# Kernel tuning notes

Measured on AMD Instinct MI355X. Metric: run time of the kernel, lower is better.

## Reference

```python
import jax, jax.numpy as jnp
import numpy as np
import math

DIMS, HEAD = 1024, 16
HD = DIMS // HEAD          # 64
B, CTX = 4, 1024
MAX_ITER, THRESH = 3, 0.5  # temp=1.0 -> q temperature scaling branch is skipped (as in torch)
LOG10_21 = math.log10(1.0 + 4000.0 / 200.0)


def _freq_angles(c):
    # compute_freqs_base: 0.2*(10**linspace(0, log10(21), d/2) - 1), custom_freqs = 36000/220 * base
    d2 = HD // 2
    mel = 10.0 ** jnp.linspace(0.0, LOG10_21, d2) - 1.0
    freqs = (36000.0 / 220.0) * (200.0 * mel / 1000.0)        # [d2]
    t = jnp.arange(c, dtype=jnp.float32)
    return t[:, None] * freqs[None, :]                          # [c, d2]


def _rope(x, ang):
    # lucidrains rotary_embedding_torch convention: interleaved pairs (x0,x1),(x2,x3),...
    x1, x2 = x[..., 0::2], x[..., 1::2]
    cos, sin = jnp.cos(ang), jnp.sin(ang)
    out = jnp.stack([x1 * cos - x2 * sin, x1 * sin + x2 * cos], axis=-1)
    return out.reshape(x.shape)


def _rms(x, w):
    eps = jnp.finfo(x.dtype).eps  # torch nn.RMSNorm eps=None default
    return x * jax.lax.rsqrt(jnp.mean(jnp.square(x), -1, keepdims=True) + eps) * w


def _sdpa(q, k, v):
    # mask is always None in this module's forward -> non-causal SDPA
    s = jnp.einsum('bhqd,bhkd->bhqk', q, k) / math.sqrt(q.shape[-1])
    return jnp.einsum('bhqk,bhkd->bhqd', jax.nn.softmax(s, -1), v)


def _focus(x, xa, P):
    # x: [b, cq, D] queries, xa: [b, ck, D] keys/values. In our configs cq == ck == eff_span.
    b, cq, D = x.shape
    ck = xa.shape[1]
    q = _rms(x, P['wq_norm']) @ P['Wq'] + P['bq']
    q = q.reshape(b, cq, HEAD, HD).transpose(0, 2, 1, 3)                 # b h c d
    kv = _rms(xa, P['wkv_norm']) @ P['Wkv'] + P['bkv']
    kv = kv.reshape(b, ck, 2, HEAD, HD).transpose(2, 0, 3, 1, 4)         # kv b h c d
    k, v = kv[0], kv[1]
    q = _rope(q, _freq_angles(cq))
    k = _rope(k, _freq_angles(ck))

    e = min(cq, ck)  # static; equals cq in all call sites here
    curq, kc, vc = q, k[:, :, :e], v[:, :, :e]
    prev = jnp.zeros_like(q)
    attn_out = jnp.zeros_like(q)
    done = jnp.asarray(False)
    for it in range(MAX_ITER):
        # torch: q/k/v re-projected from current state EVERY iteration (k,v compound)
        qp = curq[:, :, :e] @ P['Wlq'] + P['blq']
        kp = kc @ P['Wlk'] + P['blk']
        vp = vc @ P['Wlv'] + P['blv']
        attn = _sdpa(_rms(qp, P['wln']), _rms(kp, P['wln']), vp)         # == iter_out since e == cq
        diff = jnp.mean(jnp.abs(attn - prev))
        stop = (diff < THRESH) & (it > 0) & (~done)
        attn_out = jnp.where(done, attn_out, attn)  # on the break iteration attn_out = iter_out
        done = done | stop
        curq = jnp.where(done, curq, curq + attn)
        prev = jnp.where(done, prev, attn)
        kc = jnp.where(done, kc, kp)
        vc = jnp.where(done, vc, vp)
    return attn_out.transpose(0, 2, 1, 3).reshape(b, cq, D)             # b c (h d)


def _slide(x, P):
    # win_size = head_dim; only the first win_size keys of each span are ever used
    b, ctx, D = x.shape
    w = HD
    off = w // HEAD                       # span_len - win_size
    nwin = ctx // w                       # ctx chosen as a multiple of w
    starts = jnp.maximum(jnp.arange(nwin) * w - off, 0)
    kidx = starts[:, None] + jnp.arange(w)[None, :]                      # [nwin, w]
    qwin = x.reshape(b, nwin, w, D).transpose(1, 0, 2, 3)                # [nwin, b, w, D]
    kwin = x[:, kidx, :].transpose(1, 0, 2, 3)                           # [nwin, b, w, D]
    outw = jax.vmap(lambda xq, xk: _focus(xq, xk, P))(qwin, kwin)
    return outw.transpose(1, 0, 2, 3).reshape(b, ctx, D)


def _forward(x, xa, P):
    xw = _slide(x, P)
    xaw = _slide(xa, P)
    out = _focus(xw, xaw, P)
    return out @ P['Wo'] + P['bo']        # Dropout(0.01) is identity in eval


def setup_inputs() -> dict:
    key = jax.random.key(0)
    ks = jax.random.split(key, 8)
    s = 0.02
    f32 = jnp.float32
    return {
        'x': jax.random.normal(ks[0], (B, CTX, DIMS), f32),
        'xa': jax.random.normal(ks[1], (B, CTX, DIMS), f32),
        'wq_norm': jnp.ones((DIMS,), f32),
        'Wq': jax.random.normal(ks[2], (DIMS, DIMS), f32) * s,
        'bq': jnp.zeros((DIMS,), f32),
        'wkv_norm': jnp.ones((DIMS,), f32),
        'Wkv': jax.random.normal(ks[3], (DIMS, 2 * DIMS), f32) * s,
        'bkv': jnp.zeros((2 * DIMS,), f32),
        'wln': jnp.ones((HD,), f32),
        'Wlq': jax.random.normal(ks[4], (HD, HD), f32) * s,
        'blq': jnp.zeros((HD,), f32),
        'Wlk': jax.random.normal(ks[5], (HD, HD), f32) * s,
        'blk': jnp.zeros((HD,), f32),
        'Wlv': jax.random.normal(ks[6], (HD, HD), f32) * s,
        'blv': jnp.zeros((HD,), f32),
        'Wo': jax.random.normal(ks[7], (DIMS, DIMS), f32) * s,
        'bo': jnp.zeros((DIMS,), f32),
    }


def reference(x, xa, wq_norm, Wq, bq, wkv_norm, Wkv, bkv, wln, Wlq, blq, Wlk, blk, Wlv, blv, Wo, bo):
    P = dict(wq_norm=wq_norm, Wq=Wq, bq=bq, wkv_norm=wkv_norm, Wkv=Wkv, bkv=bkv, wln=wln,
             Wlq=Wlq, blq=blq, Wlk=Wlk, blk=blk, Wlv=Wlv, blv=blv, Wo=Wo, bo=bo)
    return _forward(x, xa, P)
```

## Files before the change

### kernel.cpp

```cpp
#include <hip/hip_runtime.h>
#include <math.h>

#define TPB 256

static __device__ __forceinline__ float4 mk4(float a, float b, float c, float d) {
  float4 r; r.x = a; r.y = b; r.z = c; r.w = d; return r;
}

static __device__ __forceinline__ float4 ld4s(const float* buf, int row, int ch) {
  return *(const float4*)&buf[(row << 6) + (((ch ^ (row >> 2)) & 15) << 2)];
}
static __device__ __forceinline__ void st4s(float* buf, int row, int ch, float4 v) {
  *(float4*)&buf[(row << 6) + (((ch ^ (row >> 2)) & 15) << 2)] = v;
}

__global__ __launch_bounds__(TPB) void k_tables(float* __restrict__ cosb,
                                                float* __restrict__ sinb) {
  int gid = blockIdx.x * TPB + threadIdx.x;
  if (gid >= 1024 * 32) return;
  int t = gid >> 5, j = gid & 31;
  const double Ld = 1.3222192947339193;
  float Lf = (float)Ld;
  float mlog;
  if (j == 31) {
    mlog = Lf;
  } else {
    float stepf = (float)((double)j / 31.0);
    mlog = (float)((double)Lf * (double)stepf);
  }
  float p = (float)pow(10.0, (double)mlog);
  float mel = p - 1.0f;
  float t2 = (200.0f * mel) / 1000.0f;
  float freq = 163.63636363636363f * t2;
  float ang = (float)t * freq;
  double a = (double)ang;
  cosb[gid] = (float)cos(a);
  sinb[gid] = (float)sin(a);
}

__global__ __launch_bounds__(TPB) void k_rowinv(const float* __restrict__ X,
                                                float* __restrict__ inv) {
  __shared__ float red[4];
  int row = blockIdx.x;
  int tid = threadIdx.x;
  float4 v = *(const float4*)(X + (size_t)row * 1024 + tid * 4);
  float ss = v.x * v.x + v.y * v.y + v.z * v.z + v.w * v.w;
#pragma unroll
  for (int m = 1; m < 64; m <<= 1) ss += __shfl_xor(ss, m);
  if ((tid & 63) == 0) red[tid >> 6] = ss;
  __syncthreads();
  if (tid == 0) {
    float s = ((red[0] + red[1]) + (red[2] + red[3]));
    float mm = s * (1.0f / 1024.0f) + 1.1920928955078125e-7f;
    inv[row] = (float)(1.0 / sqrt((double)mm));
  }
}

__global__ __launch_bounds__(TPB) void k_gemm128(
    const float* __restrict__ X, const float* __restrict__ inv,
    const float* __restrict__ wn, const float* __restrict__ W,
    const float* __restrict__ bias, float* __restrict__ o0,
    float* __restrict__ o1, int N, int mode) {
  __shared__ float As[16][132];
  __shared__ float Bs[16][132];
  int tid = threadIdx.x;
  int bx = blockIdx.x, by = blockIdx.y;
  int tx = tid & 15, ty = tid >> 4;
  float c[8][8];
#pragma unroll
  for (int i = 0; i < 8; ++i)
#pragma unroll
    for (int j = 0; j < 8; ++j) c[i][j] = 0.0f;

  int arow = tid >> 1;
  float sA = 1.0f;
  if (inv) sA = inv[by * 128 + arow];
  const float* Xrow = X + (size_t)(by * 128 + arow) * 1024;

  for (int k0 = 0; k0 < 1024; k0 += 16) {
#pragma unroll
    for (int u = 0; u < 2; ++u) {
      int kq = ((tid & 1) * 2 + u) * 4;
      float4 a4 = *(const float4*)(Xrow + k0 + kq);
      if (wn) {
        float4 w4 = *(const float4*)(wn + k0 + kq);
        a4.x *= w4.x; a4.y *= w4.y; a4.z *= w4.z; a4.w *= w4.w;
      }
      a4.x *= sA; a4.y *= sA; a4.z *= sA; a4.w *= sA;
      As[kq + 0][arow] = a4.x;
      As[kq + 1][arow] = a4.y;
      As[kq + 2][arow] = a4.z;
      As[kq + 3][arow] = a4.w;
    }
#pragma unroll
    for (int u = 0; u < 2; ++u) {
      int kr = tid >> 4;
      int c4 = ((tid & 15) * 2 + u) * 4;
      *(float4*)&Bs[kr][c4] =
          *(const float4*)(W + (size_t)(k0 + kr) * N + bx * 128 + c4);
    }
    __syncthreads();
#pragma unroll
    for (int kk = 0; kk < 16; ++kk) {
      float4 a0 = *(const float4*)&As[kk][ty * 4];
      float4 a1 = *(const float4*)&As[kk][64 + ty * 4];
      float4 b0 = *(const float4*)&Bs[kk][tx * 4];
      float4 b1 = *(const float4*)&Bs[kk][64 + tx * 4];
      float av[8] = {a0.x, a0.y, a0.z, a0.w, a1.x, a1.y, a1.z, a1.w};
      float bv[8] = {b0.x, b0.y, b0.z, b0.w, b1.x, b1.y, b1.z, b1.w};
#pragma unroll
      for (int i = 0; i < 8; ++i)
#pragma unroll
        for (int j = 0; j < 8; ++j) c[i][j] += av[i] * bv[j];
    }
    __syncthreads();
  }

#pragma unroll
  for (int jh = 0; jh < 2; ++jh) {
    int colbase = bx * 128 + jh * 64 + tx * 4;
    float4 bb = {0.f, 0.f, 0.f, 0.f};
    if (bias) bb = *(const float4*)(bias + colbase);
#pragma unroll
    for (int ih = 0; ih < 2; ++ih) {
#pragma unroll
      for (int i2 = 0; i2 < 4; ++i2) {
        int row = by * 128 + ih * 64 + ty * 4 + i2;
        int ci = ih * 4 + i2;
        float4 o;
        o.x = c[ci][jh * 4 + 0] + bb.x;
        o.y = c[ci][jh * 4 + 1] + bb.y;
        o.z = c[ci][jh * 4 + 2] + bb.z;
        o.w = c[ci][jh * 4 + 3] + bb.w;
        if (mode == 0) {
          *(float4*)(o0 + (size_t)row * N + colbase) = o;
        } else {
          int b = row >> 10, t = row & 1023;
          float* dst = o0;
          int cc = colbase;
          if (mode == 2 && colbase >= 1024) { dst = o1; cc = colbase - 1024; }
          int ch = cc >> 6, d = cc & 63;
          *(float4*)(dst + ((size_t)((b * 16 + ch) * 1024 + t)) * 64 + d) = o;
        }
      }
    }
  }
}

__global__ __launch_bounds__(TPB) void k_rope(float* __restrict__ A, int mask,
                                              const float* __restrict__ cosb,
                                              const float* __restrict__ sinb) {
  int gid = blockIdx.x * TPB + threadIdx.x;
  int j = gid & 31;
  int row = gid >> 5;
  int t = row & 1023;
  int aidx = ((t & mask) << 5) + j;
  float cc = cosb[aidx], sn = sinb[aidx];
  size_t base = (size_t)row * 64;
  float x1 = A[base + 2 * j], x2 = A[base + 2 * j + 1];
  A[base + 2 * j] = x1 * cc - x2 * sn;
  A[base + 2 * j + 1] = x1 * sn + x2 * cc;
}

__global__ __launch_bounds__(TPB) void k_proj(
    const float* __restrict__ curq, float* __restrict__ kc,
    float* __restrict__ vc, float* __restrict__ qph, float* __restrict__ kph,
    const float* __restrict__ Wlq, const float* __restrict__ blq,
    const float* __restrict__ Wlk, const float* __restrict__ blk,
    const float* __restrict__ Wlv, const float* __restrict__ blv,
    const float* __restrict__ wln, int CQ, const int* __restrict__ flags) {
  int RT = CQ >> 4;
  int bid = blockIdx.x;
  int rt = bid % RT;
  int rest = bid / RT;
  int h = rest & 15; rest >>= 4;
  int b = rest & 3;
  int win = rest >> 2;
  if (flags && flags[win]) return;
  __shared__ float qs[16][68], ksm[16][68], vsm[16][68];
  __shared__ float Wqs[4096], Wks[4096], Wvs[4096];
  int tid = threadIdx.x;
#pragma unroll
  for (int i = 0; i < 4; ++i) {
    int f4 = (i * 256 + tid) * 4;
    *(float4*)&Wqs[f4] = *(const float4*)(Wlq + f4);
    *(float4*)&Wks[f4] = *(const float4*)(Wlk + f4);
    *(float4*)&Wvs[f4] = *(const float4*)(Wlv + f4);
  }
  int lr = tid >> 4, c4 = (tid & 15) * 4;
  int bh = b * 16 + h;
  size_t rowbase = (size_t)bh * 1024 + (size_t)win * CQ + rt * 16;
  size_t g = (rowbase + lr) * 64 + c4;
  *(float4*)&qs[lr][c4] = *(const float4*)(curq + g);
  *(float4*)&ksm[lr][c4] = *(const float4*)(kc + g);
  *(float4*)&vsm[lr][c4] = *(const float4*)(vc + g);
  __syncthreads();
  int r = tid >> 4, cg = tid & 15;
  const float eps = 1.1920928955078125e-7f;
  float4 wl4 = *(const float4*)(wln + cg * 4);
  size_t orow = (rowbase + r) * 64 + cg * 4;
  float4 acc;
  float ssum, rms;
  acc = *(const float4*)(blq + cg * 4);
#pragma unroll 8
  for (int k = 0; k < 64; ++k) {
    float xv = qs[r][k];
    float4 w4 = *(const float4*)&Wqs[k * 64 + cg * 4];
    acc.x += xv * w4.x; acc.y += xv * w4.y;
    acc.z += xv * w4.z; acc.w += xv * w4.w;
  }
  ssum = acc.x * acc.x + acc.y * acc.y + acc.z * acc.z + acc.w * acc.w;
#pragma unroll
  for (int m = 1; m < 16; m <<= 1) ssum += __shfl_xor(ssum, m);
  rms = (float)(1.0 / sqrt((double)(ssum * 0.015625f + eps)));
  {
    float4 o;
    o.x = acc.x * rms * wl4.x; o.y = acc.y * rms * wl4.y;
    o.z = acc.z * rms * wl4.z; o.w = acc.w * rms * wl4.w;
    *(float4*)(qph + orow) = o;
  }
  acc = *(const float4*)(blk + cg * 4);
#pragma unroll 8
  for (int k = 0; k < 64; ++k) {
    float xv = ksm[r][k];
    float4 w4 = *(const float4*)&Wks[k * 64 + cg * 4];
    acc.x += xv * w4.x; acc.y += xv * w4.y;
    acc.z += xv * w4.z; acc.w += xv * w4.w;
  }
  *(float4*)(kc + orow) = acc;
  ssum = acc.x * acc.x + acc.y * acc.y + acc.z * acc.z + acc.w * acc.w;
#pragma unroll
  for (int m = 1; m < 16; m <<= 1) ssum += __shfl_xor(ssum, m);
  rms = (float)(1.0 / sqrt((double)(ssum * 0.015625f + eps)));
  {
    float4 o;
    o.x = acc.x * rms * wl4.x; o.y = acc.y * rms * wl4.y;
    o.z = acc.z * rms * wl4.z; o.w = acc.w * rms * wl4.w;
    *(float4*)(kph + orow) = o;
  }
  acc = *(const float4*)(blv + cg * 4);
#pragma unroll 8
  for (int k = 0; k < 64; ++k) {
    float xv = vsm[r][k];
    float4 w4 = *(const float4*)&Wvs[k * 64 + cg * 4];
    acc.x += xv * w4.x; acc.y += xv * w4.y;
    acc.z += xv * w4.z; acc.w += xv * w4.w;
  }
  *(float4*)(vc + orow) = acc;
}

static __device__ __forceinline__ void slide_proj_one(
    float* src, float* rawdst, float* ndst, const float* __restrict__ W,
    const float* __restrict__ bias, float4 wl4, int tx, int ty) {
  const float eps = 1.1920928955078125e-7f;
  float4 bb = *(const float4*)(bias + tx * 4);
  float4 acc[4];
#pragma unroll
  for (int i = 0; i < 4; ++i) acc[i] = bb;
#pragma unroll 2
  for (int k4 = 0; k4 < 16; ++k4) {
    const float* w = W + (k4 * 4) * 64 + tx * 4;
    float4 w0 = *(const float4*)(w);
    float4 w1 = *(const float4*)(w + 64);
    float4 w2 = *(const float4*)(w + 128);
    float4 w3 = *(const float4*)(w + 192);
#pragma unroll
    for (int i = 0; i < 4; ++i) {
      float4 a4 = ld4s(src, ty * 4 + i, k4);
      acc[i].x += a4.x * w0.x; acc[i].y += a4.x * w0.y;
      acc[i].z += a4.x * w0.z; acc[i].w += a4.x * w0.w;
      acc[i].x += a4.y * w1.x; acc[i].y += a4.y * w1.y;
      acc[i].z += a4.y * w1.z; acc[i].w += a4.y * w1.w;
      acc[i].x += a4.z * w2.x; acc[i].y += a4.z * w2.y;
      acc[i].z += a4.z * w2.z; acc[i].w += a4.z * w2.w;
      acc[i].x += a4.w * w3.x; acc[i].y += a4.w * w3.y;
      acc[i].z += a4.w * w3.z; acc[i].w += a4.w * w3.w;
    }
  }
#pragma unroll
  for (int i = 0; i < 4; ++i) {
    int row = ty * 4 + i;
    if (rawdst) st4s(rawdst, row, tx, acc[i]);
    if (ndst) {
      float ssum = acc[i].x * acc[i].x + acc[i].y * acc[i].y +
                   acc[i].z * acc[i].z + acc[i].w * acc[i].w;
#pragma unroll
      for (int mm = 1; mm < 16; mm <<= 1) ssum += __shfl_xor(ssum, mm);
      float rms = (float)(1.0 / sqrt((double)(ssum * 0.015625f + eps)));
      st4s(ndst, row, tx, mk4(acc[i].x * rms * wl4.x, acc[i].y * rms * wl4.y,
                              acc[i].z * rms * wl4.z, acc[i].w * rms * wl4.w));
    }
  }
}

__global__ __launch_bounds__(TPB) void k_slide(
    const float* __restrict__ Qg, const float* __restrict__ Kg,
    const float* __restrict__ Vg, float* __restrict__ curqg,
    float* __restrict__ kcg, float* __restrict__ vcg, float* __restrict__ outb,
    float* __restrict__ diffp, const int* __restrict__ flags,
    const float* __restrict__ cosb, const float* __restrict__ sinb,
    const float* __restrict__ Wlq, const float* __restrict__ blq,
    const float* __restrict__ Wlk, const float* __restrict__ blk,
    const float* __restrict__ Wlv, const float* __restrict__ blv,
    const float* __restrict__ wln, int mode) {
  int bid = blockIdx.x;
  int win = bid & 15, bh = bid >> 4;
  int h = bh & 15, b = bh >> 4;
  if (mode == 2 && flags[win]) return;
  __shared__ float sX[4096], sKc[4096], sVc[4096], sQp[4096], sKp[4096];
  int tid = threadIdx.x;
  int tx = tid & 15, ty = tid >> 4;
  size_t bh1024 = (size_t)bh * 1024;
  int t0 = win * 64;
  const float SCL = 0.18033688011112042f;

  if (mode == 0) {
    int sw = (win == 0) ? 0 : win * 64 - 4;
#pragma unroll
    for (int u = 0; u < 4; ++u) {
      int f4 = u * 256 + tid;
      int row = f4 >> 4, ch = f4 & 15;
      int aidx = (row << 5) + ch * 2;
      float c0 = cosb[aidx], s0 = sinb[aidx];
      float c1 = cosb[aidx + 1], s1 = sinb[aidx + 1];
      float4 q = *(const float4*)(Qg + (bh1024 + t0 + row) * 64 + ch * 4);
      st4s(sX, row, ch, mk4(q.x * c0 - q.y * s0, q.x * s0 + q.y * c0,
                            q.z * c1 - q.w * s1, q.z * s1 + q.w * c1));
      float4 k = *(const float4*)(Kg + (bh1024 + sw + row) * 64 + ch * 4);
      st4s(sKc, row, ch, mk4(k.x * c0 - k.y * s0, k.x * s0 + k.y * c0,
                             k.z * c1 - k.w * s1, k.z * s1 + k.w * c1));
      st4s(sVc, row, ch,
           *(const float4*)(Vg + (bh1024 + sw + row) * 64 + ch * 4));
    }
  } else {
#pragma unroll
    for (int u = 0; u < 4; ++u) {
      int f4 = u * 256 + tid;
      int row = f4 >> 4, ch = f4 & 15;
      size_t g = (bh1024 + t0 + row) * 64 + ch * 4;
      st4s(sX, row, ch, *(const float4*)(curqg + g));
      st4s(sKc, row, ch, *(const float4*)(kcg + g));
      st4s(sVc, row, ch, *(const float4*)(vcg + g));
    }
  }
  float4 wl4 = *(const float4*)(wln + tx * 4);
  float4 prev4[4];
  int niter = (mode == 0) ? 2 : 1;
  for (int it = 0; it < niter; ++it) {
    __syncthreads();
    slide_proj_one(sX, nullptr, sQp, Wlq, blq, wl4, tx, ty);
    slide_proj_one(sKc, sKc, sKp, Wlk, blk, wl4, tx, ty);
    slide_proj_one(sVc, sVc, nullptr, Wlv, blv, wl4, tx, ty);
    __syncthreads();
    float s4[4][4];
#pragma unroll
    for (int i = 0; i < 4; ++i)
      s4[i][0] = s4[i][1] = s4[i][2] = s4[i][3] = 0.0f;
#pragma unroll 4
    for (int d4 = 0; d4 < 16; ++d4) {
      float4 kv[4];
#pragma unroll
      for (int j = 0; j < 4; ++j) kv[j] = ld4s(sKp, tx * 4 + j, d4);
#pragma unroll
      for (int i = 0; i < 4; ++i) {
        float4 q4 = ld4s(sQp, ty * 4 + i, d4);
#pragma unroll
        for (int j = 0; j < 4; ++j) {
          s4[i][j] += q4.x * kv[j].x;
          s4[i][j] += q4.y * kv[j].y;
          s4[i][j] += q4.z * kv[j].z;
          s4[i][j] += q4.w * kv[j].w;
        }
      }
    }
    float lrow[4];
#pragma unroll
    for (int i = 0; i < 4; ++i) {
      s4[i][0] *= SCL; s4[i][1] *= SCL; s4[i][2] *= SCL; s4[i][3] *= SCL;
      float r0 = fmaxf(fmaxf(s4[i][0], s4[i][1]), fmaxf(s4[i][2], s4[i][3]));
#pragma unroll
      for (int mm = 1; mm < 16; mm <<= 1) r0 = fmaxf(r0, __shfl_xor(r0, mm));
      float rs = 0.0f;
#pragma unroll
      for (int j = 0; j < 4; ++j) {
        float pv = exp2f(s4[i][j] - r0);
        s4[i][j] = pv;
        rs += pv;
      }
#pragma unroll
      for (int mm = 1; mm < 16; mm <<= 1) rs += __shfl_xor(rs, mm);
      lrow[i] = rs;
    }
#pragma unroll
    for (int i = 0; i < 4; ++i)
      st4s(sQp, ty * 4 + i, tx, mk4(s4[i][0], s4[i][1], s4[i][2], s4[i][3]));
    float4 av[4];
#pragma unroll
    for (int i = 0; i < 4; ++i) av[i] = mk4(0.f, 0.f, 0.f, 0.f);
#pragma unroll 4
    for (int k4 = 0; k4 < 16; ++k4) {
      float4 v4[4];
#pragma unroll
      for (int kk = 0; kk < 4; ++kk) v4[kk] = ld4s(sVc, k4 * 4 + kk, tx);
#pragma unroll
      for (int i = 0; i < 4; ++i) {
        float4 p4 = ld4s(sQp, ty * 4 + i, k4);
        av[i].x += p4.x * v4[0].x; av[i].y += p4.x * v4[0].y;
        av[i].z += p4.x * v4[0].z; av[i].w += p4.x * v4[0].w;
        av[i].x += p4.y * v4[1].x; av[i].y += p4.y * v4[1].y;
        av[i].z += p4.y * v4[1].z; av[i].w += p4.y * v4[1].w;
        av[i].x += p4.z * v4[2].x; av[i].y += p4.z * v4[2].y;
        av[i].z += p4.z * v4[2].z; av[i].w += p4.z * v4[2].w;
        av[i].x += p4.w * v4[3].x; av[i].y += p4.w * v4[3].y;
        av[i].z += p4.w * v4[3].z; av[i].w += p4.w * v4[3].w;
      }
    }
#pragma unroll
    for (int i = 0; i < 4; ++i) {
      av[i].x /= lrow[i]; av[i].y /= lrow[i];
      av[i].z /= lrow[i]; av[i].w /= lrow[i];
    }
    if (mode == 0 && it == 0) {
#pragma unroll
      for (int i = 0; i < 4; ++i) {
        prev4[i] = av[i];
        int row = ty * 4 + i;
        float4 cq = ld4s(sX, row, tx);
        cq.x += av[i].x; cq.y += av[i].y; cq.z += av[i].z; cq.w += av[i].w;
        st4s(sX, row, tx, cq);
      }
    } else if (mode == 0) {
      float ds = 0.0f;
#pragma unroll
      for (int i = 0; i < 4; ++i) {
        int row = ty * 4 + i;
        ds += fabsf(av[i].x - prev4[i].x) + fabsf(av[i].y - prev4[i].y) +
              fabsf(av[i].z - prev4[i].z) + fabsf(av[i].w - prev4[i].w);
        float4 cq = ld4s(sX, row, tx);
        cq.x += av[i].x; cq.y += av[i].y; cq.z += av[i].z; cq.w += av[i].w;
        st4s(sX, row, tx, cq);
        size_t g = (bh1024 + t0 + row) * 64 + tx * 4;
        *(float4*)(curqg + g) = cq;
        *(float4*)(kcg + g) = ld4s(sKc, row, tx);
        *(float4*)(vcg + g) = ld4s(sVc, row, tx);
        size_t obase = ((size_t)b * 1024 + t0 + row) * 1024 + h * 64 + tx * 4;
        *(float4*)(outb + obase) = av[i];
      }
      __syncthreads();
      float* red = sKp;
      red[tid] = ds;
      __syncthreads();
      for (int s2 = 128; s2 > 0; s2 >>= 1) {
        if (tid < s2) red[tid] += red[tid + s2];
        __syncthreads();
      }
      if (tid == 0) diffp[bid] = red[0];
    } else {
#pragma unroll
      for (int i = 0; i < 4; ++i) {
        int row = ty * 4 + i;
        size_t obase = ((size_t)b * 1024 + t0 + row) * 1024 + h * 64 + tx * 4;
        *(float4*)(outb + obase) = av[i];
      }
    }
  }
}

__global__ __launch_bounds__(TPB, 1) void k_attn3(
    const float* __restrict__ qph, const float* __restrict__ kph,
    const float* __restrict__ vbuf, float* __restrict__ curq,
    float* __restrict__ prevb, float* __restrict__ outb,
    float* __restrict__ diffp, const int* __restrict__ flags, int NQT, int nt,
    int mode) {
  int bid = blockIdx.x;
  int qt = bid % NQT;
  int bh = bid / NQT;
  int h = bh & 15, b = bh >> 4;
  if (mode == 2 && flags[0]) return;
  __shared__ float region[24576];
  float* sQ = region;
  float* sK = region + 8192;
  float* sP = region;
  float* sV = region + 16384;
  int tid = threadIdx.x;
  int tx = tid & 15, ty = tid >> 4;
  size_t bh1024 = (size_t)bh * 1024;
  int q0 = qt * 128;

  float m[8], l[8], acc[8][4];
#pragma unroll
  for (int i = 0; i < 8; ++i) {
    m[i] = -INFINITY; l[i] = 0.0f;
    acc[i][0] = acc[i][1] = acc[i][2] = acc[i][3] = 0.0f;
  }
  const float SCL = 0.18033688011112042f;

  for (int kt = 0; kt < nt; ++kt) {
    int k0 = kt * 128;
#pragma unroll
    for (int u = 0; u < 8; ++u) {
      int f4 = u * 256 + tid;
      int row = f4 >> 4, ch = f4 & 15;
      int cp = ((ch ^ (row >> 3)) & 15) << 2;
      *(float4*)&sQ[(row << 6) + cp] =
          *(const float4*)(qph + (bh1024 + q0 + row) * 64 + ch * 4);
      *(float4*)&sK[(row << 6) + cp] =
          *(const float4*)(kph + (bh1024 + k0 + row) * 64 + ch * 4);
      *(float4*)&sV[(row << 6) + cp] =
          *(const float4*)(vbuf + (bh1024 + k0 + row) * 64 + ch * 4);
    }
    __syncthreads();
    float s[8][8];
#pragma unroll
    for (int i = 0; i < 8; ++i)
#pragma unroll
      for (int j = 0; j < 8; ++j) s[i][j] = 0.0f;
#pragma unroll 2
    for (int d4 = 0; d4 < 16; ++d4) {
      float4 kv[8];
#pragma unroll
      for (int j = 0; j < 8; ++j)
        kv[j] = *(const float4*)&sK[((tx * 8 + j) << 6) +
                                    (((d4 ^ tx) & 15) << 2)];
#pragma unroll
      for (int i = 0; i < 8; ++i) {
        float4 q4 = *(const float4*)&sQ[((ty * 8 + i) << 6) +
                                        (((d4 ^ ty) & 15) << 2)];
#pragma unroll
        for (int j = 0; j < 8; ++j) {
          s[i][j] += q4.x * kv[j].x;
          s[i][j] += q4.y * kv[j].y;
          s[i][j] += q4.z * kv[j].z;
          s[i][j] += q4.w * kv[j].w;
        }
      }
    }
#pragma unroll
    for (int i = 0; i < 8; ++i) {
#pragma unroll
      for (int j = 0; j < 8; ++j) s[i][j] *= SCL;
      float r0 = s[i][0];
#pragma unroll
      for (int j = 1; j < 8; ++j) r0 = fmaxf(r0, s[i][j]);
#pragma unroll
      for (int mm = 1; mm < 16; mm <<= 1) r0 = fmaxf(r0, __shfl_xor(r0, mm));
      float mnew = fmaxf(m[i], r0);
      float sc = exp2f(m[i] - mnew);
      float rs = 0.0f;
#pragma unroll
      for (int j = 0; j < 8; ++j) {
        float pv = exp2f(s[i][j] - mnew);
        s[i][j] = pv;
        rs += pv;
      }
#pragma unroll
      for (int mm = 1; mm < 16; mm <<= 1) rs += __shfl_xor(rs, mm);
      l[i] = l[i] * sc + rs;
      m[i] = mnew;
      acc[i][0] *= sc; acc[i][1] *= sc; acc[i][2] *= sc; acc[i][3] *= sc;
    }
    __syncthreads();
#pragma unroll
    for (int i = 0; i < 8; ++i) {
      int q = ty * 8 + i;
      *(float4*)&sP[(q << 7) + ((((2 * tx) ^ ty) & 31) << 2)] =
          mk4(s[i][0], s[i][1], s[i][2], s[i][3]);
      *(float4*)&sP[(q << 7) + ((((2 * tx + 1) ^ ty) & 31) << 2)] =
          mk4(s[i][4], s[i][5], s[i][6], s[i][7]);
    }
#pragma unroll 2
    for (int k4 = 0; k4 < 32; ++k4) {
      float4 v4[4];
#pragma unroll
      for (int kk = 0; kk < 4; ++kk) {
        int row = k4 * 4 + kk;
        v4[kk] =
            *(const float4*)&sV[(row << 6) + (((tx ^ (row >> 3)) & 15) << 2)];
      }
#pragma unroll
      for (int i = 0; i < 8; ++i) {
        float4 p4 = *(const float4*)&sP[((ty * 8 + i) << 7) +
                                        (((k4 ^ ty) & 31) << 2)];
        acc[i][0] += p4.x * v4[0].x; acc[i][1] += p4.x * v4[0].y;
        acc[i][2] += p4.x * v4[0].z; acc[i][3] += p4.x * v4[0].w;
        acc[i][0] += p4.y * v4[1].x; acc[i][1] += p4.y * v4[1].y;
        acc[i][2] += p4.y * v4[1].z; acc[i][3] += p4.y * v4[1].w;
        acc[i][0] += p4.z * v4[2].x; acc[i][1] += p4.z * v4[2].y;
        acc[i][2] += p4.z * v4[2].z; acc[i][3] += p4.z * v4[2].w;
        acc[i][0] += p4.w * v4[3].x; acc[i][1] += p4.w * v4[3].y;
        acc[i][2] += p4.w * v4[3].z; acc[i][3] += p4.w * v4[3].w;
      }
    }
    __syncthreads();
  }
  float ds = 0.0f;
#pragma unroll
  for (int i = 0; i < 8; ++i) {
    int t = q0 + ty * 8 + i;
    float4 att;
    att.x = acc[i][0] / l[i];
    att.y = acc[i][1] / l[i];
    att.z = acc[i][2] / l[i];
    att.w = acc[i][3] / l[i];
    size_t base = (bh1024 + t) * 64 + tx * 4;
    size_t obase = ((size_t)b * 1024 + t) * 1024 + h * 64 + tx * 4;
    if (mode == 0) {
      *(float4*)(prevb + base) = att;
      float4 cq = *(const float4*)(curq + base);
      cq.x += att.x; cq.y += att.y; cq.z += att.z; cq.w += att.w;
      *(float4*)(curq + base) = cq;
    } else if (mode == 1) {
      float4 pv = *(const float4*)(prevb + base);
      ds += fabsf(att.x - pv.x) + fabsf(att.y - pv.y) +
            fabsf(att.z - pv.z) + fabsf(att.w - pv.w);
      float4 cq = *(const float4*)(curq + base);
      cq.x += att.x; cq.y += att.y; cq.z += att.z; cq.w += att.w;
      *(float4*)(curq + base) = cq;
      *(float4*)(outb + obase) = att;
    } else {
      *(float4*)(outb + obase) = att;
    }
  }
  if (mode == 1) {
    __syncthreads();
    float* red = region;
    red[tid] = ds;
    __syncthreads();
    for (int s2 = 128; s2 > 0; s2 >>= 1) {
      if (tid < s2) red[tid] += red[tid + s2];
      __syncthreads();
    }
    if (tid == 0) diffp[bid] = red[0];
  }
}

__global__ __launch_bounds__(64) void k_finalize(const float* __restrict__ diffp,
                                                 int* __restrict__ flags,
                                                 int nwin, int nper,
                                                 float count) {
  int w = threadIdx.x;
  if (w < nwin) {
    float s = 0.0f;
    for (int i = 0; i < nper; ++i) s += diffp[w + i * nwin];
    flags[w] = (s / count < 0.5f) ? 1 : 0;
  }
}

extern "C" void kernel_launch(void* const* d_in, const int* in_sizes, int n_in,
                              void* d_out, int out_size, void* d_ws,
                              size_t ws_size, hipStream_t stream) {
  const float* x = (const float*)d_in[0];
  const float* xa = (const float*)d_in[1];
  const float* wqn = (const float*)d_in[2];
  const float* Wq = (const float*)d_in[3];
  const float* bq = (const float*)d_in[4];
  const float* wkvn = (const float*)d_in[5];
  const float* Wkv = (const float*)d_in[6];
  const float* bkv = (const float*)d_in[7];
  const float* wln = (const float*)d_in[8];
  const float* Wlq = (const float*)d_in[9];
  const float* blq = (const float*)d_in[10];
  const float* Wlk = (const float*)d_in[11];
  const float* blk = (const float*)d_in[12];
  const float* Wlv = (const float*)d_in[13];
  const float* blv = (const float*)d_in[14];
  const float* Wo = (const float*)d_in[15];
  const float* bo = (const float*)d_in[16];

  float* ws = (float*)d_ws;
  const size_t SLOT = (size_t)4 * 16 * 1024 * 64;
  float* xw = ws;
  float* xaw = ws + SLOT;
  float* Q = ws + 2 * SLOT;
  float* K = ws + 3 * SLOT;
  float* V = ws + 4 * SLOT;
  float* kc = ws + 5 * SLOT;
  float* vc = ws + 6 * SLOT;
  float* prev = ws + 7 * SLOT;
  float* qph = ws + 8 * SLOT;
  float* kph = ws + 9 * SLOT;
  float* misc = ws + 10 * SLOT;
  float* inv = misc;
  float* cosb = misc + 8192;
  float* sinb = cosb + 32768;
  float* diffp = sinb + 32768;
  int* flags = (int*)(diffp + 4096);

  k_tables<<<128, TPB, 0, stream>>>(cosb, sinb);

  for (int sl = 0; sl < 2; ++sl) {
    const float* Xin = sl ? xa : x;
    float* Xout = sl ? xaw : xw;
    k_rowinv<<<4096, TPB, 0, stream>>>(Xin, inv);
    k_gemm128<<<dim3(8, 32), TPB, 0, stream>>>(Xin, inv, wqn, Wq, bq, Q, nullptr, 1024, 1);
    k_gemm128<<<dim3(16, 32), TPB, 0, stream>>>(Xin, inv, wkvn, Wkv, bkv, K, V, 2048, 2);
    k_slide<<<1024, TPB, 0, stream>>>(Q, K, V, Q, kc, vc, Xout, diffp, nullptr,
                                      cosb, sinb, Wlq, blq, Wlk, blk, Wlv, blv,
                                      wln, 0);
    k_finalize<<<1, 64, 0, stream>>>(diffp, flags, 16, 64, 262144.0f);
    k_slide<<<1024, TPB, 0, stream>>>(Q, K, V, Q, kc, vc, Xout, diffp, flags,
                                      cosb, sinb, Wlq, blq, Wlk, blk, Wlv, blv,
                                      wln, 2);
  }

  k_rowinv<<<4096, TPB, 0, stream>>>(xw, inv);
  k_gemm128<<<dim3(8, 32), TPB, 0, stream>>>(xw, inv, wqn, Wq, bq, Q, nullptr, 1024, 1);
  k_rowinv<<<4096, TPB, 0, stream>>>(xaw, inv);
  k_gemm128<<<dim3(16, 32), TPB, 0, stream>>>(xaw, inv, wkvn, Wkv, bkv, K, V, 2048, 2);
  k_rope<<<8192, TPB, 0, stream>>>(Q, 1023, cosb, sinb);
  k_rope<<<8192, TPB, 0, stream>>>(K, 1023, cosb, sinb);
  float* fout = xw;
  k_proj<<<4096, TPB, 0, stream>>>(Q, K, V, qph, kph, Wlq, blq, Wlk, blk, Wlv, blv, wln, 1024, nullptr);
  k_attn3<<<512, TPB, 0, stream>>>(qph, kph, V, Q, prev, fout, diffp, nullptr, 8, 8, 0);
  k_proj<<<4096, TPB, 0, stream>>>(Q, K, V, qph, kph, Wlq, blq, Wlk, blk, Wlv, blv, wln, 1024, nullptr);
  k_attn3<<<512, TPB, 0, stream>>>(qph, kph, V, Q, prev, fout, diffp, nullptr, 8, 8, 1);
  k_finalize<<<1, 64, 0, stream>>>(diffp, flags, 1, 512, 4194304.0f);
  k_proj<<<4096, TPB, 0, stream>>>(Q, K, V, qph, kph, Wlq, blq, Wlk, blk, Wlv, blv, wln, 1024, flags);
  k_attn3<<<512, TPB, 0, stream>>>(qph, kph, V, Q, prev, fout, diffp, flags, 8, 8, 2);

  k_gemm128<<<dim3(8, 32), TPB, 0, stream>>>(fout, nullptr, nullptr, Wo, bo, (float*)d_out, nullptr, 1024, 0);
}
```

Before: 2.493 ms.

## Read Q/K/V directly from global memory in attention, keep only P in LDS

The attention kernel no longer stages Q, K and V tiles in shared memory. Each thread loads its Q rows, K rows and V columns straight from global memory through the caches, and only the softmax probability tile stays in LDS. This removes the cooperative tile loads and the block-wide barriers per key tile, and shrinks LDS use so more blocks can fit on a CU. In exchange it relies on L1/L2 hits for heavily reused, strided K/Q reads, and depends on sP reads and writes staying within a single wavefront now that the barriers are gone.

```diff
diff --git a/kernel.cpp b/kernel.cpp
--- a/kernel.cpp
+++ b/kernel.cpp
@@ -466,7 +466,7 @@
   }
 }
 
-__global__ __launch_bounds__(TPB, 1) void k_attn3(
+__global__ __launch_bounds__(TPB) void k_attn4(
     const float* __restrict__ qph, const float* __restrict__ kph,
     const float* __restrict__ vbuf, float* __restrict__ curq,
     float* __restrict__ prevb, float* __restrict__ outb,
@@ -477,15 +477,12 @@
   int bh = bid / NQT;
   int h = bh & 15, b = bh >> 4;
   if (mode == 2 && flags[0]) return;
-  __shared__ float region[24576];
-  float* sQ = region;
-  float* sK = region + 8192;
-  float* sP = region;
-  float* sV = region + 16384;
+  __shared__ float sP[128 * 128];
   int tid = threadIdx.x;
   int tx = tid & 15, ty = tid >> 4;
   size_t bh1024 = (size_t)bh * 1024;
   int q0 = qt * 128;
+  const float* Qb = qph + (bh1024 + q0 + ty * 8) * 64;
 
   float m[8], l[8], acc[8][4];
 #pragma unroll
@@ -497,35 +494,22 @@
 
   for (int kt = 0; kt < nt; ++kt) {
     int k0 = kt * 128;
-#pragma unroll
-    for (int u = 0; u < 8; ++u) {
-      int f4 = u * 256 + tid;
-      int row = f4 >> 4, ch = f4 & 15;
-      int cp = ((ch ^ (row >> 3)) & 15) << 2;
-      *(float4*)&sQ[(row << 6) + cp] =
-          *(const float4*)(qph + (bh1024 + q0 + row) * 64 + ch * 4);
-      *(float4*)&sK[(row << 6) + cp] =
-          *(const float4*)(kph + (bh1024 + k0 + row) * 64 + ch * 4);
-      *(float4*)&sV[(row << 6) + cp] =
-          *(const float4*)(vbuf + (bh1024 + k0 + row) * 64 + ch * 4);
-    }
-    __syncthreads();
+    const float* Kb = kph + (bh1024 + k0 + tx * 8) * 64;
+    const float* Vb = vbuf + (bh1024 + k0) * 64 + tx * 4;
     float s[8][8];
 #pragma unroll
     for (int i = 0; i < 8; ++i)
 #pragma unroll
       for (int j = 0; j < 8; ++j) s[i][j] = 0.0f;
-#pragma unroll 2
+#pragma unroll 4
     for (int d4 = 0; d4 < 16; ++d4) {
       float4 kv[8];
 #pragma unroll
       for (int j = 0; j < 8; ++j)
-        kv[j] = *(const float4*)&sK[((tx * 8 + j) << 6) +
-                                    (((d4 ^ tx) & 15) << 2)];
+        kv[j] = *(const float4*)(Kb + j * 64 + d4 * 4);
 #pragma unroll
       for (int i = 0; i < 8; ++i) {
-        float4 q4 = *(const float4*)&sQ[((ty * 8 + i) << 6) +
-                                        (((d4 ^ ty) & 15) << 2)];
+        float4 q4 = *(const float4*)(Qb + i * 64 + d4 * 4);
 #pragma unroll
         for (int j = 0; j < 8; ++j) {
           s[i][j] += q4.x * kv[j].x;
@@ -559,7 +543,6 @@
       m[i] = mnew;
       acc[i][0] *= sc; acc[i][1] *= sc; acc[i][2] *= sc; acc[i][3] *= sc;
     }
-    __syncthreads();
 #pragma unroll
     for (int i = 0; i < 8; ++i) {
       int q = ty * 8 + i;
@@ -572,11 +555,8 @@
     for (int k4 = 0; k4 < 32; ++k4) {
       float4 v4[4];
 #pragma unroll
-      for (int kk = 0; kk < 4; ++kk) {
-        int row = k4 * 4 + kk;
-        v4[kk] =
-            *(const float4*)&sV[(row << 6) + (((tx ^ (row >> 3)) & 15) << 2)];
-      }
+      for (int kk = 0; kk < 4; ++kk)
+        v4[kk] = *(const float4*)(Vb + (k4 * 4 + kk) * 64);
 #pragma unroll
       for (int i = 0; i < 8; ++i) {
         float4 p4 = *(const float4*)&sP[((ty * 8 + i) << 7) +
@@ -591,7 +571,6 @@
         acc[i][2] += p4.w * v4[3].z; acc[i][3] += p4.w * v4[3].w;
       }
     }
-    __syncthreads();
   }
   float ds = 0.0f;
 #pragma unroll
@@ -623,7 +602,7 @@
   }
   if (mode == 1) {
     __syncthreads();
-    float* red = region;
+    float* red = sP;
     red[tid] = ds;
     __syncthreads();
     for (int s2 = 128; s2 > 0; s2 >>= 1) {
@@ -711,12 +690,12 @@
   k_rope<<<8192, TPB, 0, stream>>>(K, 1023, cosb, sinb);
   float* fout = xw;
   k_proj<<<4096, TPB, 0, stream>>>(Q, K, V, qph, kph, Wlq, blq, Wlk, blk, Wlv, blv, wln, 1024, nullptr);
-  k_attn3<<<512, TPB, 0, stream>>>(qph, kph, V, Q, prev, fout, diffp, nullptr, 8, 8, 0);
+  k_attn4<<<512, TPB, 0, stream>>>(qph, kph, V, Q, prev, fout, diffp, nullptr, 8, 8, 0);
   k_proj<<<4096, TPB, 0, stream>>>(Q, K, V, qph, kph, Wlq, blq, Wlk, blk, Wlv, blv, wln, 1024, nullptr);
-  k_attn3<<<512, TPB, 0, stream>>>(qph, kph, V, Q, prev, fout, diffp, nullptr, 8, 8, 1);
+  k_attn4<<<512, TPB, 0, stream>>>(qph, kph, V, Q, prev, fout, diffp, nullptr, 8, 8, 1);
   k_finalize<<<1, 64, 0, stream>>>(diffp, flags, 1, 512, 4194304.0f);
   k_proj<<<4096, TPB, 0, stream>>>(Q, K, V, qph, kph, Wlq, blq, Wlk, blk, Wlv, blv, wln, 1024, flags);
-  k_attn3<<<512, TPB, 0, stream>>>(qph, kph, V, Q, prev, fout, diffp, flags, 8, 8, 2);
+  k_attn4<<<512, TPB, 0, stream>>>(qph, kph, V, Q, prev, fout, diffp, flags, 8, 8, 2);
 
   k_gemm128<<<dim3(8, 32), TPB, 0, stream>>>(fout, nullptr, nullptr, Wo, bo, (float*)d_out, nullptr, 1024, 0);
 }
```

New measurement: 2.869 ms. 15.1% more time.
